# Kernel tuning notes

Hardware: AMD Instinct MI355X
Metric: run time of the kernel (lower is better)

Reference implementation:

```python
import jax, jax.numpy as jnp
import numpy as np

D_MODEL = 768
NUM_HEADS = 12
D_K = D_MODEL // NUM_HEADS


def setup_inputs() -> dict:
    key = jax.random.key(0)
    ks = jax.random.split(key, 12)
    B, S = 4, 2048
    s = 1.0 / np.sqrt(D_MODEL)
    inp = {
        "query": jax.random.normal(ks[0], (B, S, D_MODEL), jnp.float32),
        "key": jax.random.normal(ks[1], (B, S, D_MODEL), jnp.float32),
        "value": jax.random.normal(ks[2], (B, S, D_MODEL), jnp.float32),
        "Wq": jax.random.normal(ks[3], (D_MODEL, D_MODEL), jnp.float32) * s,
        "bq": jnp.zeros((D_MODEL,), jnp.float32),
        "Wk": jax.random.normal(ks[4], (D_MODEL, D_MODEL), jnp.float32) * s,
        "bk": jnp.zeros((D_MODEL,), jnp.float32),
        "Wv": jax.random.normal(ks[5], (D_MODEL, D_MODEL), jnp.float32) * s,
        "bv": jnp.zeros((D_MODEL,), jnp.float32),
        "Wo": jax.random.normal(ks[6], (D_MODEL, D_MODEL), jnp.float32) * s,
        "bo": jnp.zeros((D_MODEL,), jnp.float32),
    }
    return inp


def _split_heads(x):
    B, S, _ = x.shape
    return x.reshape(B, S, NUM_HEADS, D_K).transpose(0, 2, 1, 3)  # [B,H,S,Dk]


def reference(query, key, value, Wq, bq, Wk, bk, Wv, bv, Wo, bo):
    # Linear projections (torch nn.Linear: x @ W.T + b)
    Q = _split_heads(query @ Wq.T + bq)
    K = _split_heads(key @ Wk.T + bk)
    V = _split_heads(value @ Wv.T + bv)
    scale = 1.0 / jnp.sqrt(jnp.asarray(D_K, Q.dtype))
    scores = jnp.einsum("bhqd,bhkd->bhqk", Q, K) * scale  # [B,H,S,S]
    attn = jax.nn.softmax(scores, axis=-1)
    # dropout is identity in eval mode
    out = jnp.einsum("bhqk,bhkd->bhqd", attn, V)  # [B,H,S,Dk]
    B, H, S, Dk = out.shape
    out = out.transpose(0, 2, 1, 3).reshape(B, S, H * Dk)
    return out @ Wo.T + bo
```

## Files before the change

kernel.cpp:

```cpp
#include <hip/hip_runtime.h>
#include <hip/hip_bf16.h>

typedef _Float16 half8 __attribute__((ext_vector_type(8)));
typedef _Float16 h4 __attribute__((ext_vector_type(4)));
typedef float f32x4 __attribute__((ext_vector_type(4)));

#define D_MODEL 768
#define NUM_HEADS 12
#define D_K 64
#define SEQ 2048
#define BATCH 4
#define M_TOTAL (BATCH * SEQ)
#define W_ELEMS (D_MODEL * D_MODEL)
#define X_ELEMS (M_TOTAL * D_MODEL)
#define QSCALE 0.18033688011112042f
#define SOFF 8.0f

__device__ __forceinline__ void gll16(const _Float16* g, _Float16* l) {
    __builtin_amdgcn_global_load_lds(
        (const __attribute__((address_space(1))) unsigned int*)g,
        (__attribute__((address_space(3))) unsigned int*)l,
        16, 0, 0);
}

__global__ void convert4(const float* __restrict__ s0, const float* __restrict__ s1,
                         const float* __restrict__ s2, const float* __restrict__ s3,
                         _Float16* __restrict__ dst, int n4) {
    const float* srcs[4] = {s0, s1, s2, s3};
    const float* s = srcs[blockIdx.y];
    _Float16* o = dst + (size_t)blockIdx.y * ((size_t)n4 * 4);
    int i = blockIdx.x * blockDim.x + threadIdx.x;
    if (i < n4) {
        float4 f = ((const float4*)s)[i];
        h4 h;
        h[0] = (_Float16)f.x; h[1] = (_Float16)f.y;
        h[2] = (_Float16)f.z; h[3] = (_Float16)f.w;
        ((h4*)o)[i] = h;
    }
}

__global__ __launch_bounds__(256) void gemm_qkv(
    const _Float16* __restrict__ Xall, const _Float16* __restrict__ Wall,
    const float* __restrict__ bq, const float* __restrict__ bk, const float* __restrict__ bv,
    _Float16* __restrict__ Qo, _Float16* __restrict__ Ko, _Float16* __restrict__ Vto)
{
    __shared__ __align__(16) char smem[36864];
    _Float16* As = (_Float16*)smem;
    _Float16* Bs = As + 128 * 64;

    const int z = blockIdx.z;
    const _Float16* X = Xall + (size_t)z * X_ELEMS;
    const _Float16* W = Wall + (size_t)z * W_ELEMS;

    const int t = threadIdx.x;
    const int w = t >> 6;
    const int l = t & 63;
    const int ln = t & 15;
    const int quad = (t >> 4) & 3;
    const int wm = w >> 1, wn = w & 1;
    const int m0 = blockIdx.x * 128, n0 = blockIdx.y * 128;

    const int srow = l >> 3;
    const int scol = (l & 7) ^ srow;

    f32x4 acc[4][4] = {};

    for (int k0 = 0; k0 < D_MODEL; k0 += 64) {
#pragma unroll
        for (int jj = 0; jj < 4; ++jj) {
            int j = w * 4 + jj;
            int row = j * 8 + srow;
            gll16(X + (size_t)(m0 + row) * D_MODEL + k0 + scol * 8, As + j * 512);
            gll16(W + (size_t)(n0 + row) * D_MODEL + k0 + scol * 8, Bs + j * 512);
        }
        __syncthreads();

#pragma unroll
        for (int kk = 0; kk < 2; ++kk) {
            half8 a[4], b[4];
#pragma unroll
            for (int i = 0; i < 4; ++i) {
                int ra = wm * 64 + i * 16 + ln;
                int rb = wn * 64 + i * 16 + ln;
                a[i] = *(const half8*)&As[ra * 64 + (((kk * 4 + quad) ^ (ln & 7)) * 8)];
                b[i] = *(const half8*)&Bs[rb * 64 + (((kk * 4 + quad) ^ (ln & 7)) * 8)];
            }
#pragma unroll
            for (int i = 0; i < 4; ++i)
#pragma unroll
                for (int j2 = 0; j2 < 4; ++j2)
                    acc[i][j2] = __builtin_amdgcn_mfma_f32_16x16x32_f16(a[i], b[j2], acc[i][j2], 0, 0, 0);
        }
        __syncthreads();
    }

    const float* bias = (z == 0) ? bq : (z == 1) ? bk : bv;
    if (z <= 1) {
        _Float16* dst = (z == 0) ? Qo : Ko;
#pragma unroll
        for (int i = 0; i < 4; ++i) {
#pragma unroll
            for (int j = 0; j < 4; ++j) {
                int n = n0 + wn * 64 + j * 16 + ln;
                int h = n >> 6, d = n & 63;
                float bn = bias[n];
#pragma unroll
                for (int r = 0; r < 4; ++r) {
                    int m = m0 + wm * 64 + i * 16 + quad * 4 + r;
                    int b_ = m >> 11, s_ = m & 2047;
                    float v = acc[i][j][r] + bn;
                    if (z == 0) v *= QSCALE;
                    dst[((size_t)((b_ * NUM_HEADS + h) * SEQ + s_)) * D_K + d] = (_Float16)v;
                }
            }
        }
    } else {
        _Float16* T = (_Float16*)smem + (size_t)w * (64 * 72);
#pragma unroll
        for (int i = 0; i < 4; ++i) {
#pragma unroll
            for (int j = 0; j < 4; ++j) {
                float bn = bias[n0 + wn * 64 + j * 16 + ln];
                h4 hh;
#pragma unroll
                for (int r = 0; r < 4; ++r) hh[r] = (_Float16)(acc[i][j][r] + bn);
                *(h4*)&T[(j * 16 + ln) * 72 + i * 16 + quad * 4] = hh;
            }
        }
        const int b_ = m0 >> 11;
        const int s0 = (m0 & 2047) + wm * 64;
        const int head = (n0 >> 6) + wn;
        _Float16* base = Vto + (size_t)(b_ * NUM_HEADS + head) * D_K * SEQ + s0;
#pragma unroll
        for (int r8 = 0; r8 < 8; ++r8) {
            int nl = r8 * 8 + (l >> 3);
            half8 v = *(const half8*)&T[nl * 72 + (l & 7) * 8];
            *(half8*)(base + (size_t)nl * SEQ + (l & 7) * 8) = v;
        }
    }
}

__global__ __launch_bounds__(256) void attn(
    const _Float16* __restrict__ Qg, const _Float16* __restrict__ Kg,
    const _Float16* __restrict__ Vtg, _Float16* __restrict__ ctx)
{
    __shared__ __align__(16) _Float16 Ks[64 * 64];
    __shared__ __align__(16) _Float16 Vs[64 * 64];

    const int t = threadIdx.x;
    const int w = t >> 6;
    const int l = t & 63;
    const int ln = t & 15;
    const int quad = (t >> 4) & 3;
    const int bh = blockIdx.y;
    const int q0 = blockIdx.x * 128 + w * 32;

    const _Float16* Qh = Qg + (size_t)bh * SEQ * D_K;
    const _Float16* Kh = Kg + (size_t)bh * SEQ * D_K;
    const _Float16* Vh = Vtg + (size_t)bh * D_K * SEQ;

    const int srow = l >> 3;
    const int scol = (l & 7) ^ srow;

    half8 qf[2][2];
#pragma unroll
    for (int qt = 0; qt < 2; ++qt)
#pragma unroll
        for (int dh = 0; dh < 2; ++dh)
            qf[qt][dh] = *(const half8*)(Qh + (size_t)(q0 + qt * 16 + ln) * D_K + dh * 32 + quad * 8);

    f32x4 acc[2][4] = {};
    f32x4 lsum[2] = {};

    for (int c = 0; c < SEQ / 64; ++c) {
        const int k0 = c * 64;
#pragma unroll
        for (int jj = 0; jj < 2; ++jj) {
            int j = w * 2 + jj;
            int row = j * 8 + srow;
            gll16(Kh + (size_t)(k0 + row) * D_K + scol * 8, Ks + j * 512);
            gll16(Vh + (size_t)row * SEQ + k0 + scol * 8, Vs + j * 512);
        }
        __syncthreads();

        h4 pB[2][4];
#pragma unroll
        for (int kt = 0; kt < 4; ++kt) {
            half8 kf0 = *(const half8*)&Ks[(kt * 16 + ln) * 64 + ((quad ^ (ln & 7)) * 8)];
            half8 kf1 = *(const half8*)&Ks[(kt * 16 + ln) * 64 + (((4 + quad) ^ (ln & 7)) * 8)];
#pragma unroll
            for (int qt = 0; qt < 2; ++qt) {
                f32x4 s = {-SOFF, -SOFF, -SOFF, -SOFF};
                s = __builtin_amdgcn_mfma_f32_16x16x32_f16(kf0, qf[qt][0], s, 0, 0, 0);
                s = __builtin_amdgcn_mfma_f32_16x16x32_f16(kf1, qf[qt][1], s, 0, 0, 0);
                f32x4 p;
                p[0] = exp2f(s[0]); p[1] = exp2f(s[1]);
                p[2] = exp2f(s[2]); p[3] = exp2f(s[3]);
                lsum[qt] += p;
                h4 h;
                h[0] = (_Float16)p[0]; h[1] = (_Float16)p[1];
                h[2] = (_Float16)p[2]; h[3] = (_Float16)p[3];
                pB[qt][kt] = h;
            }
        }

#pragma unroll
        for (int dt = 0; dt < 4; ++dt) {
#pragma unroll
            for (int kt = 0; kt < 4; ++kt) {
                int g = kt * 2 + (quad >> 1);
                h4 vf = *(const h4*)&Vs[(dt * 16 + ln) * 64 + ((g ^ (ln & 7)) * 8) + (quad & 1) * 4];
                acc[0][dt] = __builtin_amdgcn_mfma_f32_16x16x16f16(vf, pB[0][kt], acc[0][dt], 0, 0, 0);
                acc[1][dt] = __builtin_amdgcn_mfma_f32_16x16x16f16(vf, pB[1][kt], acc[1][dt], 0, 0, 0);
            }
        }
        __syncthreads();
    }

    const int h = bh % NUM_HEADS, b = bh / NUM_HEADS;
#pragma unroll
    for (int qt = 0; qt < 2; ++qt) {
        float lp = lsum[qt][0] + lsum[qt][1] + lsum[qt][2] + lsum[qt][3];
        lp += __shfl_xor(lp, 16);
        lp += __shfl_xor(lp, 32);
        float rinv = 1.0f / lp;
        int q = q0 + qt * 16 + ln;
#pragma unroll
        for (int dt = 0; dt < 4; ++dt) {
            h4 o;
            o[0] = (_Float16)(acc[qt][dt][0] * rinv);
            o[1] = (_Float16)(acc[qt][dt][1] * rinv);
            o[2] = (_Float16)(acc[qt][dt][2] * rinv);
            o[3] = (_Float16)(acc[qt][dt][3] * rinv);
            *(h4*)&ctx[((size_t)(b * SEQ + q)) * D_MODEL + h * D_K + dt * 16 + quad * 4] = o;
        }
    }
}

__global__ __launch_bounds__(256) void gemm_out(
    const _Float16* __restrict__ A, const _Float16* __restrict__ W,
    const float* __restrict__ bo, float* __restrict__ out)
{
    __shared__ __align__(16) _Float16 As[128 * 64];
    __shared__ __align__(16) _Float16 Bs[128 * 64];

    const int t = threadIdx.x;
    const int w = t >> 6;
    const int l = t & 63;
    const int ln = t & 15;
    const int quad = (t >> 4) & 3;
    const int wm = w >> 1, wn = w & 1;
    const int m0 = blockIdx.x * 128, n0 = blockIdx.y * 128;

    const int srow = l >> 3;
    const int scol = (l & 7) ^ srow;

    f32x4 acc[4][4] = {};

    for (int k0 = 0; k0 < D_MODEL; k0 += 64) {
#pragma unroll
        for (int jj = 0; jj < 4; ++jj) {
            int j = w * 4 + jj;
            int row = j * 8 + srow;
            gll16(A + (size_t)(m0 + row) * D_MODEL + k0 + scol * 8, As + j * 512);
            gll16(W + (size_t)(n0 + row) * D_MODEL + k0 + scol * 8, Bs + j * 512);
        }
        __syncthreads();

#pragma unroll
        for (int kk = 0; kk < 2; ++kk) {
            half8 a[4], b[4];
#pragma unroll
            for (int i = 0; i < 4; ++i) {
                int ra = wm * 64 + i * 16 + ln;
                int rb = wn * 64 + i * 16 + ln;
                a[i] = *(const half8*)&As[ra * 64 + (((kk * 4 + quad) ^ (ln & 7)) * 8)];
                b[i] = *(const half8*)&Bs[rb * 64 + (((kk * 4 + quad) ^ (ln & 7)) * 8)];
            }
#pragma unroll
            for (int i = 0; i < 4; ++i)
#pragma unroll
                for (int j2 = 0; j2 < 4; ++j2)
                    acc[i][j2] = __builtin_amdgcn_mfma_f32_16x16x32_f16(a[i], b[j2], acc[i][j2], 0, 0, 0);
        }
        __syncthreads();
    }

#pragma unroll
    for (int i = 0; i < 4; ++i) {
#pragma unroll
        for (int j = 0; j < 4; ++j) {
            int n = n0 + wn * 64 + j * 16 + ln;
            float bn = bo[n];
#pragma unroll
            for (int r = 0; r < 4; ++r) {
                int m = m0 + wm * 64 + i * 16 + quad * 4 + r;
                out[(size_t)m * D_MODEL + n] = acc[i][j][r] + bn;
            }
        }
    }
}

extern "C" void kernel_launch(void* const* d_in, const int* in_sizes, int n_in,
                              void* d_out, int out_size, void* d_ws, size_t ws_size,
                              hipStream_t stream) {
    const float* query = (const float*)d_in[0];
    const float* key   = (const float*)d_in[1];
    const float* value = (const float*)d_in[2];
    const float* Wq = (const float*)d_in[3];
    const float* bq = (const float*)d_in[4];
    const float* Wk = (const float*)d_in[5];
    const float* bk = (const float*)d_in[6];
    const float* Wv = (const float*)d_in[7];
    const float* bv = (const float*)d_in[8];
    const float* Wo = (const float*)d_in[9];
    const float* bo = (const float*)d_in[10];
    float* out = (float*)d_out;

    _Float16* ws = (_Float16*)d_ws;
    _Float16* Wb  = ws;
    _Float16* Xb  = Wb + 4 * (size_t)W_ELEMS;
    _Float16* Qb  = Xb + 3 * (size_t)X_ELEMS;
    _Float16* Kb  = Qb + (size_t)X_ELEMS;
    _Float16* Vtb = Kb + (size_t)X_ELEMS;
    _Float16* ctx = Vtb + (size_t)X_ELEMS;

    convert4<<<dim3(W_ELEMS / 4 / 256, 4), 256, 0, stream>>>(Wq, Wk, Wv, Wo, Wb, W_ELEMS / 4);
    convert4<<<dim3(X_ELEMS / 4 / 256, 3), 256, 0, stream>>>(query, key, value, query, Xb, X_ELEMS / 4);

    gemm_qkv<<<dim3(M_TOTAL / 128, D_MODEL / 128, 3), 256, 0, stream>>>(
        Xb, Wb, bq, bk, bv, Qb, Kb, Vtb);

    attn<<<dim3(SEQ / 128, BATCH * NUM_HEADS), 256, 0, stream>>>(Qb, Kb, Vtb, ctx);

    gemm_out<<<dim3(M_TOTAL / 128, D_MODEL / 128), 256, 0, stream>>>(
        ctx, Wb + 3 * (size_t)W_ELEMS, bo, out);
}
```

Baseline: 292.5 us.

## Double-buffer attention K/V tiles, merge convert launches, use packed fp16 convert

The attention kernel now double-buffers the K and V shared-memory tiles, issuing async global-to-LDS loads for the next chunk while the current one is computed. This is meant to hide load latency behind the MFMA work. The two fp32-to-fp16 conversion launches become one kernel, P is packed to fp16 with a cvt_pkrtz builtin, and the softmax offset constant drops from 8 to 4. Double buffering doubles the LDS footprint, which may lower occupancy. The loop appears to keep only its trailing barrier, so there may be no barrier between issuing the next loads and reading the current buffer, which risks a race and makes the new path fragile.

```diff
diff --git a/kernel.cpp b/kernel.cpp
--- a/kernel.cpp
+++ b/kernel.cpp
@@ -3,6 +3,7 @@
 
 typedef _Float16 half8 __attribute__((ext_vector_type(8)));
 typedef _Float16 h4 __attribute__((ext_vector_type(4)));
+typedef __fp16 fp16x2 __attribute__((ext_vector_type(2)));
 typedef float f32x4 __attribute__((ext_vector_type(4)));
 
 #define D_MODEL 768
@@ -14,7 +15,7 @@
 #define W_ELEMS (D_MODEL * D_MODEL)
 #define X_ELEMS (M_TOTAL * D_MODEL)
 #define QSCALE 0.18033688011112042f
-#define SOFF 8.0f
+#define SOFF 4.0f
 
 __device__ __forceinline__ void gll16(const _Float16* g, _Float16* l) {
     __builtin_amdgcn_global_load_lds(
@@ -23,20 +24,37 @@
         16, 0, 0);
 }
 
-__global__ void convert4(const float* __restrict__ s0, const float* __restrict__ s1,
-                         const float* __restrict__ s2, const float* __restrict__ s3,
-                         _Float16* __restrict__ dst, int n4) {
-    const float* srcs[4] = {s0, s1, s2, s3};
-    const float* s = srcs[blockIdx.y];
-    _Float16* o = dst + (size_t)blockIdx.y * ((size_t)n4 * 4);
-    int i = blockIdx.x * blockDim.x + threadIdx.x;
-    if (i < n4) {
-        float4 f = ((const float4*)s)[i];
-        h4 h;
-        h[0] = (_Float16)f.x; h[1] = (_Float16)f.y;
-        h[2] = (_Float16)f.z; h[3] = (_Float16)f.w;
-        ((h4*)o)[i] = h;
-    }
+__device__ __forceinline__ void pk2(float a, float b, _Float16* out) {
+    fp16x2 r = __builtin_amdgcn_cvt_pkrtz(a, b);
+    out[0] = (_Float16)r[0];
+    out[1] = (_Float16)r[1];
+}
+
+__global__ void convert_all(
+    const float* __restrict__ w0, const float* __restrict__ w1,
+    const float* __restrict__ w2, const float* __restrict__ w3,
+    const float* __restrict__ x0, const float* __restrict__ x1,
+    const float* __restrict__ x2, _Float16* __restrict__ dst)
+{
+    const size_t W4 = W_ELEMS / 4, X4 = X_ELEMS / 4;
+    size_t i = (size_t)blockIdx.x * blockDim.x + threadIdx.x;
+    const float* src;
+    size_t off;
+    if (i < 4 * W4) {
+        size_t slab = i / W4;
+        off = i - slab * W4;
+        src = (slab == 0) ? w0 : (slab == 1) ? w1 : (slab == 2) ? w2 : w3;
+    } else {
+        size_t j = i - 4 * W4;
+        size_t slab = j / X4;
+        off = j - slab * X4;
+        src = (slab == 0) ? x0 : (slab == 1) ? x1 : x2;
+    }
+    float4 f = ((const float4*)src)[off];
+    h4 h;
+    h[0] = (_Float16)f.x; h[1] = (_Float16)f.y;
+    h[2] = (_Float16)f.z; h[3] = (_Float16)f.w;
+    ((h4*)dst)[i] = h;
 }
 
 __global__ __launch_bounds__(256) void gemm_qkv(
@@ -144,8 +162,8 @@
     const _Float16* __restrict__ Qg, const _Float16* __restrict__ Kg,
     const _Float16* __restrict__ Vtg, _Float16* __restrict__ ctx)
 {
-    __shared__ __align__(16) _Float16 Ks[64 * 64];
-    __shared__ __align__(16) _Float16 Vs[64 * 64];
+    __shared__ __align__(16) _Float16 Ks[2][64 * 64];
+    __shared__ __align__(16) _Float16 Vs[2][64 * 64];
 
     const int t = threadIdx.x;
     const int w = t >> 6;
@@ -161,6 +179,11 @@
 
     const int srow = l >> 3;
     const int scol = (l & 7) ^ srow;
+    const int j0 = w * 2, j1 = w * 2 + 1;
+    const _Float16* Ksrc0 = Kh + (size_t)(j0 * 8 + srow) * D_K + scol * 8;
+    const _Float16* Ksrc1 = Kh + (size_t)(j1 * 8 + srow) * D_K + scol * 8;
+    const _Float16* Vsrc0 = Vh + (size_t)(j0 * 8 + srow) * SEQ + scol * 8;
+    const _Float16* Vsrc1 = Vh + (size_t)(j1 * 8 + srow) * SEQ + scol * 8;
 
     half8 qf[2][2];
 #pragma unroll
@@ -172,22 +195,30 @@
     f32x4 acc[2][4] = {};
     f32x4 lsum[2] = {};
 
+    gll16(Ksrc0, &Ks[0][j0 * 512]);
+    gll16(Ksrc1, &Ks[0][j1 * 512]);
+    gll16(Vsrc0, &Vs[0][j0 * 512]);
+    gll16(Vsrc1, &Vs[0][j1 * 512]);
+    __syncthreads();
+
     for (int c = 0; c < SEQ / 64; ++c) {
-        const int k0 = c * 64;
-#pragma unroll
-        for (int jj = 0; jj < 2; ++jj) {
-            int j = w * 2 + jj;
-            int row = j * 8 + srow;
-            gll16(Kh + (size_t)(k0 + row) * D_K + scol * 8, Ks + j * 512);
-            gll16(Vh + (size_t)row * SEQ + k0 + scol * 8, Vs + j * 512);
-        }
-        __syncthreads();
+        const int cur = c & 1;
+        if (c + 1 < SEQ / 64) {
+            const size_t koff = (size_t)(c + 1) * 64 * D_K;
+            const size_t voff = (size_t)(c + 1) * 64;
+            gll16(Ksrc0 + koff, &Ks[cur ^ 1][j0 * 512]);
+            gll16(Ksrc1 + koff, &Ks[cur ^ 1][j1 * 512]);
+            gll16(Vsrc0 + voff, &Vs[cur ^ 1][j0 * 512]);
+            gll16(Vsrc1 + voff, &Vs[cur ^ 1][j1 * 512]);
+        }
+        const _Float16* KsC = Ks[cur];
+        const _Float16* VsC = Vs[cur];
 
         h4 pB[2][4];
 #pragma unroll
         for (int kt = 0; kt < 4; ++kt) {
-            half8 kf0 = *(const half8*)&Ks[(kt * 16 + ln) * 64 + ((quad ^ (ln & 7)) * 8)];
-            half8 kf1 = *(const half8*)&Ks[(kt * 16 + ln) * 64 + (((4 + quad) ^ (ln & 7)) * 8)];
+            half8 kf0 = *(const half8*)&KsC[(kt * 16 + ln) * 64 + ((quad ^ (ln & 7)) * 8)];
+            half8 kf1 = *(const half8*)&KsC[(kt * 16 + ln) * 64 + (((4 + quad) ^ (ln & 7)) * 8)];
 #pragma unroll
             for (int qt = 0; qt < 2; ++qt) {
                 f32x4 s = {-SOFF, -SOFF, -SOFF, -SOFF};
@@ -198,8 +229,8 @@
                 p[2] = exp2f(s[2]); p[3] = exp2f(s[3]);
                 lsum[qt] += p;
                 h4 h;
-                h[0] = (_Float16)p[0]; h[1] = (_Float16)p[1];
-                h[2] = (_Float16)p[2]; h[3] = (_Float16)p[3];
+                pk2(p[0], p[1], (_Float16*)&h);
+                pk2(p[2], p[3], ((_Float16*)&h) + 2);
                 pB[qt][kt] = h;
             }
         }
@@ -209,7 +240,7 @@
 #pragma unroll
             for (int kt = 0; kt < 4; ++kt) {
                 int g = kt * 2 + (quad >> 1);
-                h4 vf = *(const h4*)&Vs[(dt * 16 + ln) * 64 + ((g ^ (ln & 7)) * 8) + (quad & 1) * 4];
+                h4 vf = *(const h4*)&VsC[(dt * 16 + ln) * 64 + ((g ^ (ln & 7)) * 8) + (quad & 1) * 4];
                 acc[0][dt] = __builtin_amdgcn_mfma_f32_16x16x16f16(vf, pB[0][kt], acc[0][dt], 0, 0, 0);
                 acc[1][dt] = __builtin_amdgcn_mfma_f32_16x16x16f16(vf, pB[1][kt], acc[1][dt], 0, 0, 0);
             }
@@ -325,8 +356,9 @@
     _Float16* Vtb = Kb + (size_t)X_ELEMS;
     _Float16* ctx = Vtb + (size_t)X_ELEMS;
 
-    convert4<<<dim3(W_ELEMS / 4 / 256, 4), 256, 0, stream>>>(Wq, Wk, Wv, Wo, Wb, W_ELEMS / 4);
-    convert4<<<dim3(X_ELEMS / 4 / 256, 3), 256, 0, stream>>>(query, key, value, query, Xb, X_ELEMS / 4);
+    const size_t total4 = (4 * (size_t)W_ELEMS + 3 * (size_t)X_ELEMS) / 4;
+    convert_all<<<(int)(total4 / 256), 256, 0, stream>>>(
+        Wq, Wk, Wv, Wo, query, key, value, Wb);
 
     gemm_qkv<<<dim3(M_TOTAL / 128, D_MODEL / 128, 3), 256, 0, stream>>>(
         Xb, Wb, bq, bk, bv, Qb, Kb, Vtb);
```

Result: slower. 299.8 us (+2.5%).
